# Performance work log

Measured on AMD Instinct MI355X. Metric: run time of the kernel, lower is better.

The kernel has to match this reference:

```python
import jax, jax.numpy as jnp
import numpy as np

NUM_LAYERS = 4
CODEBOOK_SIZE = 2048
DIM = 256
N = 32768
BETA = 0.25
EPS = 1e-12  # F.normalize eps


def setup_inputs() -> dict:
    key = jax.random.key(0)
    kx, kc = jax.random.split(key)
    x = jax.random.normal(kx, (N, DIM), dtype=jnp.float32)
    # nn.Embedding default init: N(0, 1)
    codebooks = jax.random.normal(kc, (NUM_LAYERS, CODEBOOK_SIZE, DIM), dtype=jnp.float32)
    return {"x": x, "codebooks": codebooks}


def reference(x, codebooks):
    sg = jax.lax.stop_gradient
    residual = x
    all_indices = []
    decoded = jnp.zeros_like(x)
    total_loss = jnp.zeros((), dtype=x.dtype)
    n_elem = x.size
    for layer in range(NUM_LAYERS):
        cb = codebooks[layer]                      # [K, D] (raw, used for gather)
        norm = jnp.linalg.norm(cb, axis=-1, keepdims=True)
        cbn = cb / jnp.maximum(norm, EPS)          # L2-normalized, used for distances
        # squared L2 distances; argmin is invariant to the sqrt in torch.cdist
        d2 = (
            jnp.sum(residual * residual, axis=-1, keepdims=True)
            - 2.0 * residual @ cbn.T
            + jnp.sum(cbn * cbn, axis=-1)
        )                                          # [N, K]
        idx = jnp.argmin(d2, axis=-1)              # [N]
        all_indices.append(idx)
        q = cb[idx]                                # [N, D] gather from RAW codebook
        codebook_loss = jnp.sum((residual - sg(q)) ** 2) / n_elem
        commitment_loss = jnp.sum((sg(residual) - q) ** 2) / n_elem
        total_loss = total_loss + codebook_loss + BETA * commitment_loss
        decoded = decoded + q
        # residual = residual - (residual + sg(q - residual)) == sg(residual - q)
        residual = sg(residual - q)
    stru_ids = jnp.stack(all_indices, axis=1)      # [N, L]
    return stru_ids, decoded, total_loss
```

## Files before the change

kernel.cpp:

```cpp
#include <hip/hip_runtime.h>
#include <math.h>

#define L_NUM 4
#define K_CB  2048
#define D_DIM 256
#define N_ROWS 32768
#define CAP 56
#define WACC  0.12f
#define WACC2 0.125f

typedef _Float16 half8 __attribute__((ext_vector_type(8)));
typedef _Float16 half4v __attribute__((ext_vector_type(4)));
typedef float f32x16 __attribute__((ext_vector_type(16)));

__device__ __forceinline__ void gl_lds16(const void* g, void* l) {
  __builtin_amdgcn_global_load_lds(
      (const __attribute__((address_space(1))) void*)g,
      (__attribute__((address_space(3))) void*)l, 16, 0, 0);
}
__device__ __forceinline__ unsigned fenc(float f) {
  unsigned u = __float_as_uint(f);
  return (u & 0x80000000u) ? ~u : (u | 0x80000000u);
}
__device__ __forceinline__ float fdec(unsigned k) {
  unsigned u = (k & 0x80000000u) ? (k ^ 0x80000000u) : ~k;
  return __uint_as_float(u);
}

__global__ __launch_bounds__(64)
void prep_all_kernel(const float* __restrict__ cb,
                     float* __restrict__ cbn,
                     _Float16* __restrict__ cb16) {
  const int b = blockIdx.x;
  const int k = b & 2047, l = b >> 11;
  const int lane = threadIdx.x;
  float4 v = reinterpret_cast<const float4*>(cb + (size_t)b * D_DIM)[lane];
  float s = v.x*v.x + v.y*v.y + v.z*v.z + v.w*v.w;
  #pragma unroll
  for (int m = 1; m < 64; m <<= 1) s += __shfl_xor(s, m, 64);
  const float den = fmaxf(sqrtf(s), 1e-12f);
  v.x /= den; v.y /= den; v.z /= den; v.w /= den;
  reinterpret_cast<float4*>(cbn + (size_t)b * D_DIM)[lane] = v;
  half4v h;
  h[0] = (_Float16)v.x; h[1] = (_Float16)v.y; h[2] = (_Float16)v.z; h[3] = (_Float16)v.w;
  const int tile = k >> 9, col = k & 511;
  const int kchunk = lane >> 3;
  const int sslot  = (lane >> 1) & 3;
  const int rem    = (lane & 1) * 4;
  const size_t off = (size_t)l * (K_CB * D_DIM)
                   + (size_t)(tile * 8 + kchunk) * 16384
                   + (size_t)sslot * 4096 + (size_t)col * 8 + rem;
  *(half4v*)(cb16 + off) = h;
}

__global__ __launch_bounds__(512, 2)
void rq_fused_kernel(const float* __restrict__ x,
                     const float* __restrict__ cb,
                     const float* __restrict__ cbn,
                     const _Float16* __restrict__ cb16,
                     float* __restrict__ out_ids,
                     float* __restrict__ out_dec,
                     double* __restrict__ dloss) {
  extern __shared__ char sm[];
  _Float16* A16   = (_Float16*)sm;
  _Float16* Bs    = (_Float16*)(sm + 65536);
  unsigned* cp    = (unsigned*)(sm + 131072);
  int*      cn    = (int*)(sm + 131072 + 128*CAP*4);
  unsigned* gmax  = (unsigned*)((char*)cn + 512);
  unsigned* bestp = (unsigned*)((char*)gmax + 512);

  const int t = threadIdx.x;
  const int wid = t >> 6, ln = t & 63;
  const int l31 = ln & 31, hl = ln >> 5;
  const int rowg = wid >> 2, colg = wid & 3;
  const int urow = t >> 2, qo = (t & 3) * 64;
  const int row0 = blockIdx.x * 128;
  const int mrow0 = rowg * 64 + l31, mrow1 = mrow0 + 32;

  float r[64];
  {
    const float4* xg = (const float4*)(x + (size_t)(row0 + urow) * D_DIM + qo);
    #pragma unroll
    for (int i = 0; i < 16; ++i) {
      const float4 a = xg[i];
      r[i*4+0]=a.x; r[i*4+1]=a.y; r[i*4+2]=a.z; r[i*4+3]=a.w;
    }
  }
  #pragma unroll
  for (int j = 0; j < 8; ++j) {
    half8 h;
    #pragma unroll
    for (int e = 0; e < 8; ++e) h[e] = (_Float16)r[j*8+e];
    const int slot = (t & 3) * 8 + j;
    *(half8*)(A16 + slot*1024 + urow*8) = h;
  }
  if (t < 128) { cn[t] = 0; gmax[t] = 0u; bestp[t] = 0u; }
  int id0 = 0, id1 = 0, id2 = 0, id3 = 0;
  double lloss = 0.0;

  #pragma unroll 1
  for (int l = 0; l < L_NUM; ++l) {
    const char* Bimg = (const char*)cb16 + (size_t)l * (K_CB * D_DIM * 2);
    {
      char* dst = (char*)Bs;
      #pragma unroll
      for (int i = 0; i < 4; ++i)
        gl_lds16(Bimg + t*16 + i*8192, dst + t*16 + i*8192);
    }
    __syncthreads();

    f32x16 acc[4][2];

    #pragma unroll 1
    for (int g = 0; g < 32; ++g) {
      if ((g & 7) == 0) {
        #pragma unroll
        for (int bi = 0; bi < 4; ++bi)
          #pragma unroll
          for (int ai = 0; ai < 2; ++ai)
            #pragma unroll
            for (int e = 0; e < 16; ++e) acc[bi][ai][e] = 0.f;
      }
      if (g < 31) {
        char* dst = (char*)Bs + ((g + 1) & 1) * 32768;
        const char* src = Bimg + (size_t)(g + 1) * 32768;
        #pragma unroll
        for (int i = 0; i < 4; ++i)
          gl_lds16(src + t*16 + i*8192, dst + t*16 + i*8192);
      }
      const _Float16* Bb = Bs + (g & 1) * 16384;
      const int cK = g & 7;
      #pragma unroll
      for (int ks2 = 0; ks2 < 2; ++ks2) {
        const int sa = cK*4 + ks2*2 + hl;
        const int sb = ks2*2 + hl;
        half8 af[2], bf[4];
        af[0] = *(const half8*)(A16 + sa*1024 + mrow0*8);
        af[1] = *(const half8*)(A16 + sa*1024 + mrow1*8);
        #pragma unroll
        for (int bi = 0; bi < 4; ++bi) {
          const int col = colg*128 + bi*32 + l31;
          bf[bi] = *(const half8*)(Bb + sb*4096 + col*8);
        }
        #pragma unroll
        for (int bi = 0; bi < 4; ++bi) {
          acc[bi][0] = __builtin_amdgcn_mfma_f32_32x32x16_f16(bf[bi], af[0], acc[bi][0], 0, 0, 0);
          acc[bi][1] = __builtin_amdgcn_mfma_f32_32x32x16_f16(bf[bi], af[1], acc[bi][1], 0, 0, 0);
        }
      }
      if ((g & 7) == 7) {
        const int ct = g >> 3;
        #pragma unroll
        for (int ai = 0; ai < 2; ++ai) {
          const int mrow = ai ? mrow1 : mrow0;
          float m = -INFINITY;
          #pragma unroll
          for (int bi = 0; bi < 4; ++bi)
            #pragma unroll
            for (int rg = 0; rg < 16; ++rg) m = fmaxf(m, acc[bi][ai][rg]);
          atomicMax(&gmax[mrow], fenc(m));
          const float thr = fdec(gmax[mrow]) - WACC;
          #pragma unroll
          for (int bi = 0; bi < 4; ++bi)
            #pragma unroll
            for (int rg = 0; rg < 16; ++rg) {
              const float v = acc[bi][ai][rg];
              if (v >= thr) {
                const unsigned q = (unsigned)((v + 64.f) * 16384.f);
                const unsigned cidx = (unsigned)(ct*512 + colg*128 + bi*32
                                                 + 4*hl + (rg & 3) + 8*(rg >> 2));
                const unsigned pk = (q << 11) | cidx;
                atomicMax(&bestp[mrow], pk);
                const int slot = atomicAdd(&cn[mrow], 1);
                if (slot < CAP) cp[mrow*CAP + slot] = pk;
              }
            }
        }
      }
      __syncthreads();
    }

    {
      const float thr2 = fdec(gmax[urow]) - WACC2;
      const int m = min(cn[urow], CAP);
      double bsc = (double)INFINITY; int bidx = 0x7fffffff;
      #pragma unroll 1
      for (int j = 0; j <= m; ++j) {
        const unsigned p = (j < m) ? cp[urow*CAP + j] : bestp[urow];
        const float v = (float)(p >> 11) * (1.f/16384.f) - 64.f;
        if (j < m && v < thr2) continue;
        const int cidx = (int)(p & 2047u);
        const float4* cpn = (const float4*)(cbn + ((size_t)l*K_CB + cidx)*D_DIM + qo);
        double s = 0.0, n2 = 0.0;
        #pragma unroll
        for (int i = 0; i < 16; ++i) {
          const float4 a = cpn[i];
          s  = fma((double)r[i*4+0], (double)a.x, s);
          s  = fma((double)r[i*4+1], (double)a.y, s);
          s  = fma((double)r[i*4+2], (double)a.z, s);
          s  = fma((double)r[i*4+3], (double)a.w, s);
          n2 = fma((double)a.x, (double)a.x, n2);
          n2 = fma((double)a.y, (double)a.y, n2);
          n2 = fma((double)a.z, (double)a.z, n2);
          n2 = fma((double)a.w, (double)a.w, n2);
        }
        s  += __shfl_xor(s, 1, 64);  s  += __shfl_xor(s, 2, 64);
        n2 += __shfl_xor(n2, 1, 64); n2 += __shfl_xor(n2, 2, 64);
        const double sc = -2.0 * s + n2;
        if (sc < bsc || (sc == bsc && cidx < bidx)) { bsc = sc; bidx = cidx; }
      }
      bidx &= 2047;
      if (l == 0) id0 = bidx; else if (l == 1) id1 = bidx;
      else if (l == 2) id2 = bidx; else id3 = bidx;
      if ((t & 3) == 0) out_ids[(size_t)(row0 + urow)*L_NUM + l] = (float)bidx;

      const float4* qg = (const float4*)(cb + ((size_t)l*K_CB + bidx)*D_DIM + qo);
      #pragma unroll
      for (int i = 0; i < 16; ++i) {
        const float4 q = qg[i];
        r[i*4+0] -= q.x; r[i*4+1] -= q.y; r[i*4+2] -= q.z; r[i*4+3] -= q.w;
        lloss += (double)r[i*4+0]*r[i*4+0] + (double)r[i*4+1]*r[i*4+1]
               + (double)r[i*4+2]*r[i*4+2] + (double)r[i*4+3]*r[i*4+3];
      }
      if (l < 3) {
        #pragma unroll
        for (int j = 0; j < 8; ++j) {
          half8 h;
          #pragma unroll
          for (int e = 0; e < 8; ++e) h[e] = (_Float16)r[j*8+e];
          const int slot = (t & 3) * 8 + j;
          *(half8*)(A16 + slot*1024 + urow*8) = h;
        }
      }
    }
    __syncthreads();
    if (l < 3 && t < 128) { cn[t] = 0; gmax[t] = 0u; bestp[t] = 0u; }
  }

  {
    float dec[64];
    #pragma unroll
    for (int l2 = 0; l2 < L_NUM; ++l2) {
      const int idl = (l2 == 0) ? id0 : (l2 == 1) ? id1 : (l2 == 2) ? id2 : id3;
      const float4* qg = (const float4*)(cb + ((size_t)l2*K_CB + idl)*D_DIM + qo);
      #pragma unroll
      for (int i = 0; i < 16; ++i) {
        const float4 q = qg[i];
        if (l2 == 0) { dec[i*4+0]=q.x; dec[i*4+1]=q.y; dec[i*4+2]=q.z; dec[i*4+3]=q.w; }
        else { dec[i*4+0]+=q.x; dec[i*4+1]+=q.y; dec[i*4+2]+=q.z; dec[i*4+3]+=q.w; }
      }
    }
    float4* dg = (float4*)(out_dec + (size_t)(row0 + urow)*D_DIM + qo);
    #pragma unroll
    for (int i = 0; i < 16; ++i)
      dg[i] = make_float4(dec[i*4+0], dec[i*4+1], dec[i*4+2], dec[i*4+3]);
  }

  double* lw = (double*)cp;
  #pragma unroll
  for (int m = 1; m < 64; m <<= 1) lloss += __shfl_xor(lloss, m, 64);
  if (ln == 0) lw[wid] = lloss;
  __syncthreads();
  if (t == 0) {
    double s2 = 0.0;
    #pragma unroll
    for (int j = 0; j < 8; ++j) s2 += lw[j];
    atomicAdd(dloss, s2);
  }
}

__global__ void rq_fin_kernel(const double* __restrict__ dls, float* __restrict__ out_loss) {
  out_loss[0] = (float)(dls[0] * 1.25 / 8388608.0);
}

extern "C" void kernel_launch(void* const* d_in, const int* in_sizes, int n_in,
                              void* d_out, int out_size, void* d_ws, size_t ws_size,
                              hipStream_t stream) {
  const float* x  = (const float*)d_in[0];
  const float* cb = (const float*)d_in[1];
  float* out      = (float*)d_out;
  float* out_ids  = out;
  float* out_dec  = out + (size_t)N_ROWS * L_NUM;
  float* out_loss = out_dec + (size_t)N_ROWS * D_DIM;

  char* w = (char*)d_ws;
  double* dls = (double*)w;                   w += 256;
  float* cbn = (float*)w;                     w += (size_t)L_NUM*K_CB*D_DIM*4;
  _Float16* cb16 = (_Float16*)w;              w += (size_t)L_NUM*K_CB*D_DIM*2;

  hipMemsetAsync(dls, 0, sizeof(double), stream);
  prep_all_kernel<<<L_NUM*K_CB, 64, 0, stream>>>(cb, cbn, cb16);

  const size_t smem = 65536 + 65536 + 128*CAP*4 + 512 + 512 + 512;
  hipFuncSetAttribute(reinterpret_cast<const void*>(rq_fused_kernel),
                      hipFuncAttributeMaxDynamicSharedMemorySize, (int)smem);
  rq_fused_kernel<<<N_ROWS/128, 512, smem, stream>>>(x, cb, cbn, cb16,
                                                     out_ids, out_dec, dls);
  rq_fin_kernel<<<1, 1, 0, stream>>>(dls, out_loss);
}
```

Measured before the change: 345.1 us.

## Precompute codebook norms, tree-reduce tile max, prefetch next layer's first tile

Computes the double-precision squared norm of each normalized codebook row once in the prep kernel, so the candidate rescoring loop no longer recomputes it per candidate. The per-row max over accumulators becomes a balanced tree reduction instead of a serial fmax chain. The first B tile of the next layer is issued into LDS before the rescoring phase, overlapping that load with the fp64 candidate work. These are separate ideas; the prefetch relies on the tile buffer not being read during rescoring, and the change adds a small workspace array.

```diff
diff --git a/kernel.cpp b/kernel.cpp
--- a/kernel.cpp
+++ b/kernel.cpp
@@ -27,9 +27,23 @@
   return __uint_as_float(u);
 }
 
+__device__ __forceinline__ float tmax64(const f32x16& a, const f32x16& b,
+                                        const f32x16& c, const f32x16& d) {
+  float m[16];
+  #pragma unroll
+  for (int i = 0; i < 16; ++i)
+    m[i] = fmaxf(fmaxf(a[i], b[i]), fmaxf(c[i], d[i]));
+  #pragma unroll
+  for (int s2 = 8; s2 >= 1; s2 >>= 1)
+    #pragma unroll
+    for (int i = 0; i < s2; ++i) m[i] = fmaxf(m[i], m[i + s2]);
+  return m[0];
+}
+
 __global__ __launch_bounds__(64)
 void prep_all_kernel(const float* __restrict__ cb,
                      float* __restrict__ cbn,
+                     double* __restrict__ c2d,
                      _Float16* __restrict__ cb16) {
   const int b = blockIdx.x;
   const int k = b & 2047, l = b >> 11;
@@ -41,6 +55,10 @@
   const float den = fmaxf(sqrtf(s), 1e-12f);
   v.x /= den; v.y /= den; v.z /= den; v.w /= den;
   reinterpret_cast<float4*>(cbn + (size_t)b * D_DIM)[lane] = v;
+  double td = (double)v.x*v.x + (double)v.y*v.y + (double)v.z*v.z + (double)v.w*v.w;
+  #pragma unroll
+  for (int m = 1; m < 64; m <<= 1) td += __shfl_xor(td, m, 64);
+  if (lane == 0) c2d[b] = td;
   half4v h;
   h[0] = (_Float16)v.x; h[1] = (_Float16)v.y; h[2] = (_Float16)v.z; h[3] = (_Float16)v.w;
   const int tile = k >> 9, col = k & 511;
@@ -57,6 +75,7 @@
 void rq_fused_kernel(const float* __restrict__ x,
                      const float* __restrict__ cb,
                      const float* __restrict__ cbn,
+                     const double* __restrict__ c2d,
                      const _Float16* __restrict__ cb16,
                      float* __restrict__ out_ids,
                      float* __restrict__ out_dec,
@@ -98,15 +117,16 @@
   int id0 = 0, id1 = 0, id2 = 0, id3 = 0;
   double lloss = 0.0;
 
+  {
+    const char* B0 = (const char*)cb16;
+    #pragma unroll
+    for (int i = 0; i < 4; ++i)
+      gl_lds16(B0 + t*16 + i*8192, (char*)Bs + t*16 + i*8192);
+  }
+
   #pragma unroll 1
   for (int l = 0; l < L_NUM; ++l) {
     const char* Bimg = (const char*)cb16 + (size_t)l * (K_CB * D_DIM * 2);
-    {
-      char* dst = (char*)Bs;
-      #pragma unroll
-      for (int i = 0; i < 4; ++i)
-        gl_lds16(Bimg + t*16 + i*8192, dst + t*16 + i*8192);
-    }
     __syncthreads();
 
     f32x16 acc[4][2];
@@ -153,11 +173,8 @@
         #pragma unroll
         for (int ai = 0; ai < 2; ++ai) {
           const int mrow = ai ? mrow1 : mrow0;
-          float m = -INFINITY;
-          #pragma unroll
-          for (int bi = 0; bi < 4; ++bi)
-            #pragma unroll
-            for (int rg = 0; rg < 16; ++rg) m = fmaxf(m, acc[bi][ai][rg]);
+          const float m = ai ? tmax64(acc[0][1], acc[1][1], acc[2][1], acc[3][1])
+                             : tmax64(acc[0][0], acc[1][0], acc[2][0], acc[3][0]);
           atomicMax(&gmax[mrow], fenc(m));
           const float thr = fdec(gmax[mrow]) - WACC;
           #pragma unroll
@@ -180,6 +197,13 @@
       __syncthreads();
     }
 
+    if (l < 3) {
+      const char* Bn = (const char*)cb16 + (size_t)(l + 1) * (K_CB * D_DIM * 2);
+      #pragma unroll
+      for (int i = 0; i < 4; ++i)
+        gl_lds16(Bn + t*16 + i*8192, (char*)Bs + t*16 + i*8192);
+    }
+
     {
       const float thr2 = fdec(gmax[urow]) - WACC2;
       const int m = min(cn[urow], CAP);
@@ -191,22 +215,18 @@
         if (j < m && v < thr2) continue;
         const int cidx = (int)(p & 2047u);
         const float4* cpn = (const float4*)(cbn + ((size_t)l*K_CB + cidx)*D_DIM + qo);
-        double s = 0.0, n2 = 0.0;
+        double s = 0.0;
         #pragma unroll
         for (int i = 0; i < 16; ++i) {
           const float4 a = cpn[i];
-          s  = fma((double)r[i*4+0], (double)a.x, s);
-          s  = fma((double)r[i*4+1], (double)a.y, s);
-          s  = fma((double)r[i*4+2], (double)a.z, s);
-          s  = fma((double)r[i*4+3], (double)a.w, s);
-          n2 = fma((double)a.x, (double)a.x, n2);
-          n2 = fma((double)a.y, (double)a.y, n2);
-          n2 = fma((double)a.z, (double)a.z, n2);
-          n2 = fma((double)a.w, (double)a.w, n2);
-        }
-        s  += __shfl_xor(s, 1, 64);  s  += __shfl_xor(s, 2, 64);
-        n2 += __shfl_xor(n2, 1, 64); n2 += __shfl_xor(n2, 2, 64);
-        const double sc = -2.0 * s + n2;
+          s = fma((double)r[i*4+0], (double)a.x, s);
+          s = fma((double)r[i*4+1], (double)a.y, s);
+          s = fma((double)r[i*4+2], (double)a.z, s);
+          s = fma((double)r[i*4+3], (double)a.w, s);
+        }
+        s += __shfl_xor(s, 1, 64);
+        s += __shfl_xor(s, 2, 64);
+        const double sc = -2.0 * s + c2d[l*K_CB + cidx];
         if (sc < bsc || (sc == bsc && cidx < bidx)) { bsc = sc; bidx = cidx; }
       }
       bidx &= 2047;
@@ -285,16 +305,17 @@
 
   char* w = (char*)d_ws;
   double* dls = (double*)w;                   w += 256;
+  double* c2d = (double*)w;                   w += (size_t)L_NUM*K_CB*8;
   float* cbn = (float*)w;                     w += (size_t)L_NUM*K_CB*D_DIM*4;
   _Float16* cb16 = (_Float16*)w;              w += (size_t)L_NUM*K_CB*D_DIM*2;
 
   hipMemsetAsync(dls, 0, sizeof(double), stream);
-  prep_all_kernel<<<L_NUM*K_CB, 64, 0, stream>>>(cb, cbn, cb16);
+  prep_all_kernel<<<L_NUM*K_CB, 64, 0, stream>>>(cb, cbn, c2d, cb16);
 
   const size_t smem = 65536 + 65536 + 128*CAP*4 + 512 + 512 + 512;
   hipFuncSetAttribute(reinterpret_cast<const void*>(rq_fused_kernel),
                       hipFuncAttributeMaxDynamicSharedMemorySize, (int)smem);
-  rq_fused_kernel<<<N_ROWS/128, 512, smem, stream>>>(x, cb, cbn, cb16,
+  rq_fused_kernel<<<N_ROWS/128, 512, smem, stream>>>(x, cb, cbn, c2d, cb16,
                                                      out_ids, out_dec, dls);
   rq_fin_kernel<<<1, 1, 0, stream>>>(dls, out_loss);
 }
```

New measurement: 351.2 us. Within noise of the previous version (+1.8%).
